# Optimization experiments

Measured on AMD Instinct MI355X. Metric: run time of the kernel, lower is better.

## Reference

```python
import jax, jax.numpy as jnp
import numpy as np
import math

B, C, W, H = 4, 96, 64, 64
MID, OUT = 24, 256
EPS = 1e-5


def setup_inputs() -> dict:
    key = jax.random.key(0)
    ks = jax.random.split(key, 8)
    s = lambda *sh: 1.0 / math.sqrt(sh[-1])
    return {
        "rgb": jax.random.normal(ks[0], (B, C, W, H), dtype=jnp.float32),
        "dep": jax.random.normal(ks[1], (B, C, W, H), dtype=jnp.float32),
        "Wd": jax.random.normal(ks[2], (C, C), dtype=jnp.float32) * s(C, C),   # dept 1x1 conv
        "Wr": jax.random.normal(ks[3], (C, C), dtype=jnp.float32) * s(C, C),   # rgb 1x1 conv
        "Wm1": jax.random.normal(ks[4], (MID, C), dtype=jnp.float32) * s(MID, C),
        "bn1_g": jnp.ones((MID,), dtype=jnp.float32),
        "bn1_b": jnp.zeros((MID,), dtype=jnp.float32),
        "Wm2": jax.random.normal(ks[5], (OUT, MID), dtype=jnp.float32) * s(OUT, MID),
        "bn2_g": jnp.ones((OUT,), dtype=jnp.float32),
        "bn2_b": jnp.zeros((OUT,), dtype=jnp.float32),
    }


def _bn_relu(x, gamma, beta):
    # training-mode BatchNorm over batch dim (spatial is 1x1), biased variance, then ReLU
    mu = x.mean(axis=0)
    var = x.var(axis=0)
    y = (x - mu) * jax.lax.rsqrt(var + EPS) * gamma + beta
    return jax.nn.relu(y)


def reference(rgb, dep, Wd, Wr, Wm1, bn1_g, bn1_b, Wm2, bn2_g, bn2_b):
    b, c, w, h = rgb.shape
    hw = w * h
    rgbd = rgb + dep
    # 1x1 convs as channel matmuls -> [B, C, HW]
    pr = jnp.einsum('oc,bchw->bohw', Wr, rgb).reshape(b, c, hw)
    pd = jnp.einsum('oc,bchw->bohw', Wd, dep).reshape(b, c, hw)
    # energy[b, n, m] = proj_rgb^T proj_dep / sqrt(C)   -> [B, HW, HW]
    energy = jnp.einsum('bcn,bcm->bnm', pr, pd) / math.sqrt(c)
    # torch Softmax(dim=1) on [B, HW, HW] normalizes over the first HW axis
    att = jax.nn.softmax(energy, axis=1)
    att_r = jnp.einsum('bcn,bnm->bcm', pr, att)
    att_b = jnp.einsum('bcn,bnm->bcm', pd, att)
    out = (att_r + att_b).reshape(b, c, w, h) + rgbd
    gap = out.mean(axis=(2, 3))  # [B, C] (AdaptiveAvgPool2d(1) squeezed)
    h1 = _bn_relu(gap @ Wm1.T, bn1_g, bn1_b)        # [B, 24]
    gate = _bn_relu(h1 @ Wm2.T, bn2_g, bn2_b)       # [B, OUT] (ReLU, as in source)
    return gate[:, :, None, None]                    # [B, OUT, 1, 1]
```

## Files before the change

### kernel.cpp

```cpp
#include <hip/hip_runtime.h>

#define HW 4096
#define NC 96
#define NB 4
#define MID 24
#define NOUT 256
#define BEPS 1e-5f
#define SCALE2E 0.14724920341279385f

typedef unsigned short u16;
typedef short bf16x8 __attribute__((ext_vector_type(8)));
typedef unsigned short u16x8 __attribute__((ext_vector_type(8)));
typedef float f32x16 __attribute__((ext_vector_type(16)));

#define NZERO (2 * NB * HW + 16)

__device__ __forceinline__ u16 bfh(float x) {
  unsigned u = __float_as_uint(x);
  return (u16)((u + 0x7FFFu + ((u >> 16) & 1u)) >> 16);
}

__launch_bounds__(256)
__global__ void k_prep(const float* __restrict__ rgb, const float* __restrict__ dep,
                       const float* __restrict__ Wr, const float* __restrict__ Wd,
                       float* __restrict__ psum, u16* __restrict__ prF, u16* __restrict__ pdF,
                       float* __restrict__ zeroreg) {
  const int tid = threadIdx.x;
  const int lane = tid & 63;
  const int og = __builtin_amdgcn_readfirstlane(tid >> 6);
  const int b = blockIdx.y, q = blockIdx.z;
  const int n = blockIdx.x * 64 + lane;
  const int obase = q * 32 + og * 8;

  const int gtid = ((blockIdx.z * gridDim.y + blockIdx.y) * gridDim.x + blockIdx.x) * 256 + tid;
  if (gtid < NZERO) zeroreg[gtid] = 0.f;

  float ar[8], ad[8];
  #pragma unroll
  for (int o = 0; o < 8; ++o) { ar[o] = 0.f; ad[o] = 0.f; }

  const float* rb = rgb + (size_t)b * NC * HW + n;
  const float* db = dep + (size_t)b * NC * HW + n;
  #pragma unroll 4
  for (int c = 0; c < NC; ++c) {
    float xr = rb[(size_t)c * HW];
    float xd = db[(size_t)c * HW];
    #pragma unroll
    for (int o = 0; o < 8; ++o) {
      float wr = Wr[(obase + o) * NC + c];
      float wd = Wd[(obase + o) * NC + c];
      ar[o] = fmaf(wr, xr, ar[o]);
      ad[o] = fmaf(wd, xd, ad[o]);
    }
  }

  #pragma unroll
  for (int o = 0; o < 8; ++o)
    psum[((size_t)b * NC + obase + o) * HW + n] = ar[o] + ad[o];

  const int c8 = q * 4 + og;
  const int ks = c8 >> 1, khalf = c8 & 1;
  const int tile = n >> 5;
  const size_t off = (size_t)b * HW * 96
                   + ((size_t)(tile * 6 + ks) << 9) + ((khalf * 32 + (n & 31)) << 3);
  u16x8 vr, vd;
  #pragma unroll
  for (int o = 0; o < 8; ++o) { vr[o] = bfh(ar[o]); vd[o] = bfh(ad[o]); }
  *(u16x8*)(prF + off) = vr;
  *(u16x8*)(pdF + off) = vd;
}

template <int PASS>
__launch_bounds__(256, 2)
__global__ void k_energy(const u16* __restrict__ At, const u16* __restrict__ Bt,
                         const float* __restrict__ Zin, float* __restrict__ outv) {
  __shared__ float red[2][128];
  __shared__ float nlzL[128];
  const int tid = threadIdx.x;
  const int lane = tid & 63, wid = tid >> 6;
  const int wA = wid >> 1, wB = wid & 1;
  const int b = blockIdx.z;
  const int flat = blockIdx.y * 32 + blockIdx.x;
  const int by = (flat & 7) * 4 + ((flat >> 3) & 3);
  const int bx = flat >> 5;
  const int a0 = by * 128;
  const int c0 = bx * 128;
  const u16* Ab = At + (size_t)b * HW * 96;
  const u16* Bb = Bt + (size_t)b * HW * 96;
  const int tA0 = by * 4 + wA * 2;
  const int tB0 = bx * 4 + wB * 2;

  if (PASS) {
    if (tid < 128)
      nlzL[tid] = -__log2f(Zin[(size_t)b * HW + a0 + tid]);
    __syncthreads();
  }

  bf16x8 Ah[2][6];
  #pragma unroll
  for (int ta = 0; ta < 2; ++ta)
    #pragma unroll
    for (int ks = 0; ks < 6; ++ks)
      Ah[ta][ks] = *(const bf16x8*)(Ab + (((tA0 + ta) * 6 + ks) << 9) + (lane << 3));

  f32x16 acc[2][2];
  #pragma unroll
  for (int ta = 0; ta < 2; ++ta)
    #pragma unroll
    for (int tb = 0; tb < 2; ++tb)
      #pragma unroll
      for (int q = 0; q < 16; ++q) acc[ta][tb][q] = 0.f;

  #pragma unroll
  for (int ks = 0; ks < 6; ++ks) {
    #pragma unroll
    for (int tb = 0; tb < 2; ++tb) {
      bf16x8 bh = *(const bf16x8*)(Bb + (((tB0 + tb) * 6 + ks) << 9) + (lane << 3));
      #pragma unroll
      for (int ta = 0; ta < 2; ++ta)
        acc[ta][tb] = __builtin_amdgcn_mfma_f32_32x32x16_bf16(Ah[ta][ks], bh, acc[ta][tb], 0, 0, 0);
    }
  }

  float csum[2] = {0.f, 0.f};
  float nlzv = 0.f;
  if (PASS) nlzv = nlzL[wA * 64 + lane];
  #pragma unroll
  for (int ta = 0; ta < 2; ++ta) {
    #pragma unroll
    for (int q = 0; q < 16; ++q) {
      float bias = 0.f;
      if (PASS) {
        int src = ta * 32 + (q & 3) + 8 * (q >> 2) + 4 * (lane >> 5);
        bias = __shfl(nlzv, src, 64);
      }
      #pragma unroll
      for (int tb = 0; tb < 2; ++tb)
        csum[tb] += exp2f(fmaf(acc[ta][tb][q], SCALE2E, bias));
    }
  }
  #pragma unroll
  for (int tb = 0; tb < 2; ++tb) csum[tb] += __shfl_xor(csum[tb], 32, 64);
  if (lane < 32) {
    #pragma unroll
    for (int tb = 0; tb < 2; ++tb) red[wA][wB * 64 + tb * 32 + lane] = csum[tb];
  }
  __syncthreads();
  if (tid < 128)
    atomicAdd(&outv[(size_t)b * HW + c0 + tid], red[0][tid] + red[1][tid]);
}

__launch_bounds__(256)
__global__ void k_gap(const float* __restrict__ psum, const float* __restrict__ rgb,
                      const float* __restrict__ dep, const float* __restrict__ sv,
                      float* __restrict__ gapb, int* __restrict__ counter,
                      const float* __restrict__ Wm1, const float* __restrict__ g1,
                      const float* __restrict__ b1,
                      const float* __restrict__ Wm2, const float* __restrict__ g2,
                      const float* __restrict__ b2, float* __restrict__ out) {
  const int c = blockIdx.x, b = blockIdx.y;
  const int tid = threadIdx.x;
  const size_t off = ((size_t)b * NC + c) * HW;
  const float* pp = psum + off;
  const float* rp = rgb + off;
  const float* dp = dep + off;
  const float* sp = sv + (size_t)b * HW;
  float a1 = 0.f, a2 = 0.f;
  for (int n = tid * 4; n < HW; n += 1024) {
    float4 p = *(const float4*)&pp[n];
    float4 s4 = *(const float4*)&sp[n];
    float4 r4 = *(const float4*)&rp[n];
    float4 d4 = *(const float4*)&dp[n];
    a1 += p.x * s4.x + p.y * s4.y + p.z * s4.z + p.w * s4.w;
    a2 += (r4.x + d4.x) + (r4.y + d4.y) + (r4.z + d4.z) + (r4.w + d4.w);
  }
  #pragma unroll
  for (int o = 32; o > 0; o >>= 1) {
    a1 += __shfl_down(a1, o, 64);
    a2 += __shfl_down(a2, o, 64);
  }
  __shared__ float r1[4], r2[4];
  __shared__ int isLast;
  const int wv = tid >> 6;
  if ((tid & 63) == 0) { r1[wv] = a1; r2[wv] = a2; }
  __syncthreads();
  if (tid == 0) {
    float t1 = r1[0] + r1[1] + r1[2] + r1[3];
    float t2 = r2[0] + r2[1] + r2[2] + r2[3];
    gapb[b * NC + c] = (t1 + t2) * (1.0f / HW);
    __threadfence();
    int old = atomicAdd(counter, 1);
    isLast = (old == NC * NB - 1);
  }
  __syncthreads();
  if (!isLast) return;

  __shared__ float gl[NB * NC];
  __shared__ float h[NB * MID];
  __shared__ float h1r[NB * MID];
  __shared__ float h2[NB * NOUT];
  __threadfence();
  for (int i = tid; i < NB * NC; i += 256)
    gl[i] = atomicAdd(&gapb[i], 0.0f);
  __syncthreads();

  if (tid < NB * MID) {
    int bb2 = tid / MID, j = tid % MID;
    float acc = 0.f;
    #pragma unroll
    for (int cc = 0; cc < NC; ++cc) acc += gl[bb2 * NC + cc] * Wm1[j * NC + cc];
    h[bb2 * MID + j] = acc;
  }
  __syncthreads();

  if (tid < MID) {
    float x0 = h[0 * MID + tid], x1 = h[1 * MID + tid];
    float x2 = h[2 * MID + tid], x3 = h[3 * MID + tid];
    float mu = 0.25f * (x0 + x1 + x2 + x3);
    float d0 = x0 - mu, d1 = x1 - mu, d2 = x2 - mu, d3 = x3 - mu;
    float v = 0.25f * (d0 * d0 + d1 * d1 + d2 * d2 + d3 * d3);
    float sc = g1[tid] * rsqrtf(v + BEPS);
    float bb = b1[tid];
    h1r[0 * MID + tid] = fmaxf(d0 * sc + bb, 0.f);
    h1r[1 * MID + tid] = fmaxf(d1 * sc + bb, 0.f);
    h1r[2 * MID + tid] = fmaxf(d2 * sc + bb, 0.f);
    h1r[3 * MID + tid] = fmaxf(d3 * sc + bb, 0.f);
  }
  __syncthreads();

  for (int idx = tid; idx < NB * NOUT; idx += 256) {
    int bb2 = idx >> 8, o = idx & 255;
    float acc = 0.f;
    #pragma unroll
    for (int j = 0; j < MID; ++j) acc += h1r[bb2 * MID + j] * Wm2[o * MID + j];
    h2[bb2 * NOUT + o] = acc;
  }
  __syncthreads();

  if (tid < NOUT) {
    float x0 = h2[0 * NOUT + tid], x1 = h2[1 * NOUT + tid];
    float x2 = h2[2 * NOUT + tid], x3 = h2[3 * NOUT + tid];
    float mu = 0.25f * (x0 + x1 + x2 + x3);
    float d0 = x0 - mu, d1 = x1 - mu, d2 = x2 - mu, d3 = x3 - mu;
    float v = 0.25f * (d0 * d0 + d1 * d1 + d2 * d2 + d3 * d3);
    float sc = g2[tid] * rsqrtf(v + BEPS);
    float bb = b2[tid];
    out[0 * NOUT + tid] = fmaxf(d0 * sc + bb, 0.f);
    out[1 * NOUT + tid] = fmaxf(d1 * sc + bb, 0.f);
    out[2 * NOUT + tid] = fmaxf(d2 * sc + bb, 0.f);
    out[3 * NOUT + tid] = fmaxf(d3 * sc + bb, 0.f);
  }
}

extern "C" void kernel_launch(void* const* d_in, const int* in_sizes, int n_in,
                              void* d_out, int out_size, void* d_ws, size_t ws_size,
                              hipStream_t stream) {
  const float* rgb   = (const float*)d_in[0];
  const float* dep   = (const float*)d_in[1];
  const float* Wd    = (const float*)d_in[2];
  const float* Wr    = (const float*)d_in[3];
  const float* Wm1   = (const float*)d_in[4];
  const float* bn1_g = (const float*)d_in[5];
  const float* bn1_b = (const float*)d_in[6];
  const float* Wm2   = (const float*)d_in[7];
  const float* bn2_g = (const float*)d_in[8];
  const float* bn2_b = (const float*)d_in[9];
  float* out = (float*)d_out;

  char* w = (char*)d_ws;
  u16* prF = (u16*)w;             w += (size_t)NB * HW * 96 * 2;
  u16* pdF = (u16*)w;             w += (size_t)NB * HW * 96 * 2;
  float* psum = (float*)w;        w += (size_t)NB * NC * HW * 4;
  float* Z    = (float*)w;        w += (size_t)NB * HW * 4;
  float* sv   = (float*)w;        w += (size_t)NB * HW * 4;
  int* counter = (int*)w;         w += 64;
  float* gap  = (float*)w;        w += (size_t)NB * NC * 4;

  k_prep<<<dim3(HW / 64, NB, 3), 256, 0, stream>>>(rgb, dep, Wr, Wd, psum, prF, pdF, Z);
  k_energy<0><<<dim3(32, 32, NB), 256, 0, stream>>>(prF, pdF, nullptr, Z);
  k_energy<1><<<dim3(32, 32, NB), 256, 0, stream>>>(pdF, prF, Z, sv);
  k_gap<<<dim3(NC, NB), 256, 0, stream>>>(psum, rgb, dep, sv, gap, counter,
                                          Wm1, bn1_g, bn1_b, Wm2, bn2_g, bn2_b, out);
}
```

Before: 97.90 us.

## Replace energy atomics with per-row-tile partial buffers and separate reduction

```diff
diff --git a/kernel.cpp b/kernel.cpp
--- a/kernel.cpp
+++ b/kernel.cpp
@@ -13,8 +13,6 @@
 typedef unsigned short u16x8 __attribute__((ext_vector_type(8)));
 typedef float f32x16 __attribute__((ext_vector_type(16)));
 
-#define NZERO (2 * NB * HW + 16)
-
 __device__ __forceinline__ u16 bfh(float x) {
   unsigned u = __float_as_uint(x);
   return (u16)((u + 0x7FFFu + ((u >> 16) & 1u)) >> 16);
@@ -24,7 +22,7 @@
 __global__ void k_prep(const float* __restrict__ rgb, const float* __restrict__ dep,
                        const float* __restrict__ Wr, const float* __restrict__ Wd,
                        float* __restrict__ psum, u16* __restrict__ prF, u16* __restrict__ pdF,
-                       float* __restrict__ zeroreg) {
+                       int* __restrict__ counter) {
   const int tid = threadIdx.x;
   const int lane = tid & 63;
   const int og = __builtin_amdgcn_readfirstlane(tid >> 6);
@@ -32,8 +30,8 @@
   const int n = blockIdx.x * 64 + lane;
   const int obase = q * 32 + og * 8;
 
-  const int gtid = ((blockIdx.z * gridDim.y + blockIdx.y) * gridDim.x + blockIdx.x) * 256 + tid;
-  if (gtid < NZERO) zeroreg[gtid] = 0.f;
+  if (blockIdx.x == 0 && blockIdx.y == 0 && blockIdx.z == 0 && tid == 0)
+    *counter = 0;
 
   float ar[8], ad[8];
   #pragma unroll
@@ -71,9 +69,9 @@
 }
 
 template <int PASS>
-__launch_bounds__(256, 2)
+__launch_bounds__(256, 3)
 __global__ void k_energy(const u16* __restrict__ At, const u16* __restrict__ Bt,
-                         const float* __restrict__ Zin, float* __restrict__ outv) {
+                         const float* __restrict__ zin, float* __restrict__ part) {
   __shared__ float red[2][128];
   __shared__ float nlzL[128];
   const int tid = threadIdx.x;
@@ -91,17 +89,14 @@
   const int tB0 = bx * 4 + wB * 2;
 
   if (PASS) {
-    if (tid < 128)
-      nlzL[tid] = -__log2f(Zin[(size_t)b * HW + a0 + tid]);
+    if (tid < 128) {
+      float s = 0.f;
+      #pragma unroll
+      for (int t = 0; t < 32; ++t) s += zin[((size_t)t * NB + b) * HW + a0 + tid];
+      nlzL[tid] = -__log2f(s);
+    }
     __syncthreads();
   }
-
-  bf16x8 Ah[2][6];
-  #pragma unroll
-  for (int ta = 0; ta < 2; ++ta)
-    #pragma unroll
-    for (int ks = 0; ks < 6; ++ks)
-      Ah[ta][ks] = *(const bf16x8*)(Ab + (((tA0 + ta) * 6 + ks) << 9) + (lane << 3));
 
   f32x16 acc[2][2];
   #pragma unroll
@@ -113,13 +108,14 @@
 
   #pragma unroll
   for (int ks = 0; ks < 6; ++ks) {
-    #pragma unroll
-    for (int tb = 0; tb < 2; ++tb) {
-      bf16x8 bh = *(const bf16x8*)(Bb + (((tB0 + tb) * 6 + ks) << 9) + (lane << 3));
-      #pragma unroll
-      for (int ta = 0; ta < 2; ++ta)
-        acc[ta][tb] = __builtin_amdgcn_mfma_f32_32x32x16_bf16(Ah[ta][ks], bh, acc[ta][tb], 0, 0, 0);
-    }
+    bf16x8 a0v = *(const bf16x8*)(Ab + (((tA0 + 0) * 6 + ks) << 9) + (lane << 3));
+    bf16x8 a1v = *(const bf16x8*)(Ab + (((tA0 + 1) * 6 + ks) << 9) + (lane << 3));
+    bf16x8 b0v = *(const bf16x8*)(Bb + (((tB0 + 0) * 6 + ks) << 9) + (lane << 3));
+    bf16x8 b1v = *(const bf16x8*)(Bb + (((tB0 + 1) * 6 + ks) << 9) + (lane << 3));
+    acc[0][0] = __builtin_amdgcn_mfma_f32_32x32x16_bf16(a0v, b0v, acc[0][0], 0, 0, 0);
+    acc[1][0] = __builtin_amdgcn_mfma_f32_32x32x16_bf16(a1v, b0v, acc[1][0], 0, 0, 0);
+    acc[0][1] = __builtin_amdgcn_mfma_f32_32x32x16_bf16(a0v, b1v, acc[0][1], 0, 0, 0);
+    acc[1][1] = __builtin_amdgcn_mfma_f32_32x32x16_bf16(a1v, b1v, acc[1][1], 0, 0, 0);
   }
 
   float csum[2] = {0.f, 0.f};
@@ -147,7 +143,15 @@
   }
   __syncthreads();
   if (tid < 128)
-    atomicAdd(&outv[(size_t)b * HW + c0 + tid], red[0][tid] + red[1][tid]);
+    part[((size_t)by * NB + b) * HW + c0 + tid] = red[0][tid] + red[1][tid];
+}
+
+__global__ void k_sred(const float* __restrict__ spart, float* __restrict__ sv) {
+  int idx = blockIdx.x * 256 + threadIdx.x;
+  float a = 0.f;
+  #pragma unroll
+  for (int t = 0; t < 32; ++t) a += spart[(size_t)t * (NB * HW) + idx];
+  sv[idx] = a;
 }
 
 __launch_bounds__(256)
@@ -270,15 +274,17 @@
   char* w = (char*)d_ws;
   u16* prF = (u16*)w;             w += (size_t)NB * HW * 96 * 2;
   u16* pdF = (u16*)w;             w += (size_t)NB * HW * 96 * 2;
-  float* psum = (float*)w;        w += (size_t)NB * NC * HW * 4;
-  float* Z    = (float*)w;        w += (size_t)NB * HW * 4;
-  float* sv   = (float*)w;        w += (size_t)NB * HW * 4;
+  float* psum  = (float*)w;       w += (size_t)NB * NC * HW * 4;
+  float* zpart = (float*)w;       w += (size_t)32 * NB * HW * 4;
+  float* spart = (float*)w;       w += (size_t)32 * NB * HW * 4;
+  float* sv    = (float*)w;       w += (size_t)NB * HW * 4;
+  float* gap   = (float*)w;       w += (size_t)NB * NC * 4;
   int* counter = (int*)w;         w += 64;
-  float* gap  = (float*)w;        w += (size_t)NB * NC * 4;
-
-  k_prep<<<dim3(HW / 64, NB, 3), 256, 0, stream>>>(rgb, dep, Wr, Wd, psum, prF, pdF, Z);
-  k_energy<0><<<dim3(32, 32, NB), 256, 0, stream>>>(prF, pdF, nullptr, Z);
-  k_energy<1><<<dim3(32, 32, NB), 256, 0, stream>>>(pdF, prF, Z, sv);
+
+  k_prep<<<dim3(HW / 64, NB, 3), 256, 0, stream>>>(rgb, dep, Wr, Wd, psum, prF, pdF, counter);
+  k_energy<0><<<dim3(32, 32, NB), 256, 0, stream>>>(prF, pdF, nullptr, zpart);
+  k_energy<1><<<dim3(32, 32, NB), 256, 0, stream>>>(pdF, prF, zpart, spart);
+  k_sred<<<NB * HW / 256, 256, 0, stream>>>(spart, sv);
   k_gap<<<dim3(NC, NB), 256, 0, stream>>>(psum, rgb, dep, sv, gap, counter,
                                           Wm1, bn1_g, bn1_b, Wm2, bn2_g, bn2_b, out);
 }
```

Result: slower. 101.4 us (+3.6%).
